# Kernel optimization log

Hardware: AMD Instinct MI355X
Metric: run time of the kernel (lower is better)

The kernel has to match this reference:

```python
import jax, jax.numpy as jnp
import numpy as np

BS, Q, K, NT = 16, 1500, 256, 150   # batch, queries, classes, GT per image (T = BS*NT)
COST_CLASS, COST_BBOX, COST_GIOU = 1.0, 5.0, 2.0
ALPHA, GAMMA, EPS = 0.25, 2.0, 1e-8


def box_cxcywh_to_xyxy(b):
    cx, cy, w, h = b[..., 0], b[..., 1], b[..., 2], b[..., 3]
    return jnp.stack([cx - 0.5 * w, cy - 0.5 * h, cx + 0.5 * w, cy + 0.5 * h], axis=-1)


def generalized_box_iou(boxes1, boxes2):
    # boxes in xyxy; boxes1: [N,4], boxes2: [M,4] -> [N,M]
    area1 = (boxes1[:, 2] - boxes1[:, 0]) * (boxes1[:, 3] - boxes1[:, 1])
    area2 = (boxes2[:, 2] - boxes2[:, 0]) * (boxes2[:, 3] - boxes2[:, 1])
    lt = jnp.maximum(boxes1[:, None, :2], boxes2[None, :, :2])
    rb = jnp.minimum(boxes1[:, None, 2:], boxes2[None, :, 2:])
    wh = jnp.clip(rb - lt, 0.0)
    inter = wh[..., 0] * wh[..., 1]
    union = area1[:, None] + area2[None, :] - inter
    iou = inter / union
    # smallest enclosing box
    lt_e = jnp.minimum(boxes1[:, None, :2], boxes2[None, :, :2])
    rb_e = jnp.maximum(boxes1[:, None, 2:], boxes2[None, :, 2:])
    wh_e = jnp.clip(rb_e - lt_e, 0.0)
    area_e = wh_e[..., 0] * wh_e[..., 1]
    return iou - (area_e - union) / area_e


def setup_inputs() -> dict:
    key = jax.random.key(0)
    k1, k2, k3, k4 = jax.random.split(key, 4)
    pred_logits = jax.random.normal(k1, (BS, Q, K), dtype=jnp.float32)
    pred_boxes = jax.random.uniform(k2, (BS, Q, 4), dtype=jnp.float32, minval=0.05, maxval=0.95)
    tgt_bbox = jax.random.uniform(k3, (BS * NT, 4), dtype=jnp.float32, minval=0.05, maxval=0.95)
    tgt_ids = jax.random.randint(k4, (BS * NT,), 0, K)
    return {"pred_logits": pred_logits, "pred_boxes": pred_boxes,
            "tgt_bbox": tgt_bbox, "tgt_ids": tgt_ids}


def reference(pred_logits, pred_boxes, tgt_bbox, tgt_ids):
    bs, nq, k = pred_logits.shape
    out_prob = jax.nn.sigmoid(pred_logits.reshape(bs * nq, k))   # [N, K]
    out_bbox = pred_boxes.reshape(bs * nq, 4)                    # [N, 4]

    # focal-style classification cost, gathered at target class columns
    neg_cost = (1.0 - ALPHA) * out_prob ** GAMMA * -jnp.log(1.0 - out_prob + EPS)
    pos_cost = ALPHA * (1.0 - out_prob) ** GAMMA * -jnp.log(out_prob + EPS)
    cost_class = (pos_cost - neg_cost)[:, tgt_ids]               # [N, T]

    # L1 box cost (cdist p=1)
    cost_bbox = jnp.sum(jnp.abs(out_bbox[:, None, :] - tgt_bbox[None, :, :]), axis=-1)

    # negative GIoU cost
    cost_giou = -generalized_box_iou(box_cxcywh_to_xyxy(out_bbox),
                                     box_cxcywh_to_xyxy(tgt_bbox))

    C = COST_BBOX * cost_bbox + COST_CLASS * cost_class + COST_GIOU * cost_giou
    return C.reshape(bs, nq, -1)                                  # [bs, Q, T]
```

## Files before the change

kernel.cpp:

```cpp
#include <hip/hip_runtime.h>
#include <cmath>


namespace {
constexpr int kBS = 16, kQ = 1500, kK = 256, kNT = 150;
constexpr int kT  = kBS * kNT;
constexpr int kN  = kBS * kQ;
constexpr int kNPB = 8;
constexpr int kGroups = 3;
constexpr float kAlpha = 0.25f;
constexpr float kEps   = 1e-8f;
}

__global__ __launch_bounds__(256)
void matcher_cost_kernel(const float* __restrict__ logits,
                         const float* __restrict__ pboxes,
                         const float* __restrict__ tboxes,
                         const int*   __restrict__ tids,
                         float* __restrict__ out)
{
    __shared__ float s_cls[kK];
    const int tid = threadIdx.x;
    const int n0  = blockIdx.x * kNPB;

    float tcx[kGroups][4], tcy[kGroups][4], twd[kGroups][4], tht[kGroups][4];
    int   tcl[kGroups][4];
    bool  valid[kGroups];
    const float4* tb4 = reinterpret_cast<const float4*>(tboxes);
    const int4*   ti4 = reinterpret_cast<const int4*>(tids);
#pragma unroll
    for (int g = 0; g < kGroups; ++g) {
        const int q4 = tid + 256 * g;
        valid[g] = (q4 < kT / 4);
        if (valid[g]) {
#pragma unroll
            for (int e = 0; e < 4; ++e) {
                const float4 b = tb4[q4 * 4 + e];
                tcx[g][e] = b.x; tcy[g][e] = b.y; twd[g][e] = b.z; tht[g][e] = b.w;
            }
            const int4 c = ti4[q4];
            tcl[g][0] = c.x; tcl[g][1] = c.y; tcl[g][2] = c.z; tcl[g][3] = c.w;
        }
    }

    for (int i = 0; i < kNPB; ++i) {
        const int n = n0 + i;

        const float x   = logits[n * kK + tid];
        const float p   = __builtin_amdgcn_rcpf(1.0f + __expf(-x));
        const float omp = 1.0f - p;
        const float ccls = -kAlpha * omp * omp * __logf(p + kEps)
                         + (1.0f - kAlpha) * p * p * __logf(omp + kEps);

        __syncthreads();
        s_cls[tid] = ccls;

        const float pcx = pboxes[n * 4 + 0];
        const float pcy = pboxes[n * 4 + 1];
        const float pw  = pboxes[n * 4 + 2];
        const float ph  = pboxes[n * 4 + 3];
        const float px1 = pcx - 0.5f * pw, py1 = pcy - 0.5f * ph;
        const float px2 = pcx + 0.5f * pw, py2 = pcy + 0.5f * ph;
        const float parea = pw * ph;

        __syncthreads();

        float4* orow = reinterpret_cast<float4*>(out + (size_t)n * kT);
#pragma unroll
        for (int g = 0; g < kGroups; ++g) {
            if (!valid[g]) continue;
            float res[4];
#pragma unroll
            for (int e = 0; e < 4; ++e) {
                const float bcx = tcx[g][e], bcy = tcy[g][e];
                const float bw  = twd[g][e], bh  = tht[g][e];

                const float cb = fabsf(pcx - bcx) + fabsf(pcy - bcy)
                               + fabsf(pw - bw)  + fabsf(ph - bh);

                const float tx1 = bcx - 0.5f * bw, ty1 = bcy - 0.5f * bh;
                const float tx2 = bcx + 0.5f * bw, ty2 = bcy + 0.5f * bh;
                const float tarea = bw * bh;
                const float iw = fmaxf(fminf(px2, tx2) - fmaxf(px1, tx1), 0.0f);
                const float ih = fmaxf(fminf(py2, ty2) - fmaxf(py1, ty1), 0.0f);
                const float inter = iw * ih;
                const float uni   = parea + tarea - inter;
                const float ew = fmaxf(fmaxf(px2, tx2) - fminf(px1, tx1), 0.0f);
                const float eh = fmaxf(fmaxf(py2, ty2) - fminf(py1, ty1), 0.0f);
                const float earea = ew * eh;
                const float iou  = inter * __builtin_amdgcn_rcpf(uni);
                const float giou = iou - (earea - uni) * __builtin_amdgcn_rcpf(earea);

                const float cc = s_cls[tcl[g][e]];
                res[e] = 5.0f * cb + cc - 2.0f * giou;
            }
            const float4 v = make_float4(res[0], res[1], res[2], res[3]);
            orow[tid + 256 * g] = v;
        }
    }
}

extern "C" void kernel_launch(void* const* d_in, const int* in_sizes, int n_in,
                              void* d_out, int out_size, void* d_ws, size_t ws_size,
                              hipStream_t stream) {
    const float* logits = (const float*)d_in[0];
    const float* pboxes = (const float*)d_in[1];
    const float* tboxes = (const float*)d_in[2];
    const int*   tids   = (const int*)d_in[3];
    float* out = (float*)d_out;

    dim3 grid(kN / kNPB);
    dim3 block(256);
    hipLaunchKernelGGL(matcher_cost_kernel, grid, block, 0, stream,
                       logits, pboxes, tboxes, tids, out);
}
```

Before: 299.7 us.

## Tile targets into LDS, batch query class costs in fp16, simplify GIoU math

```diff
diff --git a/kernel.cpp b/kernel.cpp
--- a/kernel.cpp
+++ b/kernel.cpp
@@ -1,4 +1,5 @@
 #include <hip/hip_runtime.h>
+#include <hip/hip_fp16.h>
 #include <cmath>
 
 
@@ -6,96 +7,86 @@
 constexpr int kBS = 16, kQ = 1500, kK = 256, kNT = 150;
 constexpr int kT  = kBS * kNT;
 constexpr int kN  = kBS * kQ;
-constexpr int kNPB = 8;
-constexpr int kGroups = 3;
+constexpr int kQB = 16;
+constexpr int kTT = 1024;
+constexpr int kTiles = 3;
 constexpr float kAlpha = 0.25f;
 constexpr float kEps   = 1e-8f;
 }
 
-__global__ __launch_bounds__(256)
+__global__ __launch_bounds__(256, 4)
 void matcher_cost_kernel(const float* __restrict__ logits,
                          const float* __restrict__ pboxes,
                          const float* __restrict__ tboxes,
                          const int*   __restrict__ tids,
                          float* __restrict__ out)
 {
-    __shared__ float s_cls[kK];
-    const int tid = threadIdx.x;
-    const int n0  = blockIdx.x * kNPB;
+    __shared__ float2 s_cxy[kTT];
+    __shared__ float2 s_wh[kTT];
+    __shared__ unsigned char s_cid[kTT];
+    __shared__ __half s_fcl[kQB][kK];
 
-    float tcx[kGroups][4], tcy[kGroups][4], twd[kGroups][4], tht[kGroups][4];
-    int   tcl[kGroups][4];
-    bool  valid[kGroups];
+    const int tid  = threadIdx.x;
+    const int n0   = blockIdx.x * kQB;
+    const int t0   = blockIdx.y * kTT;
+    const int tsz  = min(kTT, kT - t0);
+
     const float4* tb4 = reinterpret_cast<const float4*>(tboxes);
-    const int4*   ti4 = reinterpret_cast<const int4*>(tids);
-#pragma unroll
-    for (int g = 0; g < kGroups; ++g) {
-        const int q4 = tid + 256 * g;
-        valid[g] = (q4 < kT / 4);
-        if (valid[g]) {
-#pragma unroll
-            for (int e = 0; e < 4; ++e) {
-                const float4 b = tb4[q4 * 4 + e];
-                tcx[g][e] = b.x; tcy[g][e] = b.y; twd[g][e] = b.z; tht[g][e] = b.w;
-            }
-            const int4 c = ti4[q4];
-            tcl[g][0] = c.x; tcl[g][1] = c.y; tcl[g][2] = c.z; tcl[g][3] = c.w;
-        }
+    for (int j = tid; j < tsz; j += 256) {
+        const float4 b = tb4[t0 + j];
+        s_cxy[j] = make_float2(b.x, b.y);
+        s_wh[j]  = make_float2(b.z, b.w);
+        s_cid[j] = (unsigned char)tids[t0 + j];
     }
 
-    for (int i = 0; i < kNPB; ++i) {
-        const int n = n0 + i;
-
-        const float x   = logits[n * kK + tid];
+    for (int q = 0; q < kQB; ++q) {
+        const float x   = logits[(n0 + q) * kK + tid];
         const float p   = __builtin_amdgcn_rcpf(1.0f + __expf(-x));
         const float omp = 1.0f - p;
-        const float ccls = -kAlpha * omp * omp * __logf(p + kEps)
-                         + (1.0f - kAlpha) * p * p * __logf(omp + kEps);
+        const float cc  = -kAlpha * omp * omp * __logf(p + kEps)
+                        + (1.0f - kAlpha) * p * p * __logf(omp + kEps);
+        s_fcl[q][tid] = __float2half(cc);
+    }
 
-        __syncthreads();
-        s_cls[tid] = ccls;
+    __syncthreads();
 
+    for (int q = 0; q < kQB; ++q) {
+        const int n = n0 + q;
         const float pcx = pboxes[n * 4 + 0];
         const float pcy = pboxes[n * 4 + 1];
         const float pw  = pboxes[n * 4 + 2];
         const float ph  = pboxes[n * 4 + 3];
-        const float px1 = pcx - 0.5f * pw, py1 = pcy - 0.5f * ph;
-        const float px2 = pcx + 0.5f * pw, py2 = pcy + 0.5f * ph;
+        const float px1 = pcx - 0.5f * pw, px2 = pcx + 0.5f * pw;
+        const float py1 = pcy - 0.5f * ph, py2 = pcy + 0.5f * ph;
         const float parea = pw * ph;
+        float* __restrict__ row = out + (size_t)n * kT + t0;
 
-        __syncthreads();
+        auto body = [&](int t) {
+            const float2 cxy = s_cxy[t];
+            const float2 wh  = s_wh[t];
+            const float bcx = cxy.x, bcy = cxy.y, bw = wh.x, bh = wh.y;
+            const float cc = __half2float(s_fcl[q][s_cid[t]]);
+            const float cb = fabsf(pcx - bcx) + fabsf(pcy - bcy)
+                           + fabsf(pw - bw)  + fabsf(ph - bh);
+            const float tx1 = bcx - 0.5f * bw, tx2 = bcx + 0.5f * bw;
+            const float ty1 = bcy - 0.5f * bh, ty2 = bcy + 0.5f * bh;
+            const float ow = fminf(px2, tx2) - fmaxf(px1, tx1);
+            const float oh = fminf(py2, ty2) - fmaxf(py1, ty1);
+            const float iw = fmaxf(ow, 0.0f), ih = fmaxf(oh, 0.0f);
+            const float ew = (pw + bw) - ow,  eh = (ph + bh) - oh;
+            const float inter = iw * ih;
+            const float uni   = parea + bw * bh - inter;
+            const float earea = ew * eh;
+            const float r    = __builtin_amdgcn_rcpf(uni * earea);
+            const float frac = fmaf(uni, uni, inter * earea) * r;
+            row[t] = fmaf(5.0f, cb, cc + 2.0f) - 2.0f * frac;
+        };
 
-        float4* orow = reinterpret_cast<float4*>(out + (size_t)n * kT);
+        if (tsz == kTT) {
 #pragma unroll
-        for (int g = 0; g < kGroups; ++g) {
-            if (!valid[g]) continue;
-            float res[4];
-#pragma unroll
-            for (int e = 0; e < 4; ++e) {
-                const float bcx = tcx[g][e], bcy = tcy[g][e];
-                const float bw  = twd[g][e], bh  = tht[g][e];
-
-                const float cb = fabsf(pcx - bcx) + fabsf(pcy - bcy)
-                               + fabsf(pw - bw)  + fabsf(ph - bh);
-
-                const float tx1 = bcx - 0.5f * bw, ty1 = bcy - 0.5f * bh;
-                const float tx2 = bcx + 0.5f * bw, ty2 = bcy + 0.5f * bh;
-                const float tarea = bw * bh;
-                const float iw = fmaxf(fminf(px2, tx2) - fmaxf(px1, tx1), 0.0f);
-                const float ih = fmaxf(fminf(py2, ty2) - fmaxf(py1, ty1), 0.0f);
-                const float inter = iw * ih;
-                const float uni   = parea + tarea - inter;
-                const float ew = fmaxf(fmaxf(px2, tx2) - fminf(px1, tx1), 0.0f);
-                const float eh = fmaxf(fmaxf(py2, ty2) - fminf(py1, ty1), 0.0f);
-                const float earea = ew * eh;
-                const float iou  = inter * __builtin_amdgcn_rcpf(uni);
-                const float giou = iou - (earea - uni) * __builtin_amdgcn_rcpf(earea);
-
-                const float cc = s_cls[tcl[g][e]];
-                res[e] = 5.0f * cb + cc - 2.0f * giou;
-            }
-            const float4 v = make_float4(res[0], res[1], res[2], res[3]);
-            orow[tid + 256 * g] = v;
+            for (int e = 0; e < 4; ++e) body(tid + 256 * e);
+        } else {
+            for (int t = tid; t < tsz; t += 256) body(t);
         }
     }
 }
@@ -109,7 +100,7 @@
     const int*   tids   = (const int*)d_in[3];
     float* out = (float*)d_out;
 
-    dim3 grid(kN / kNPB);
+    dim3 grid(kN / kQB, kTiles);
     dim3 block(256);
     hipLaunchKernelGGL(matcher_cost_kernel, grid, block, 0, stream,
                        logits, pboxes, tboxes, tids, out);
```

New measurement: 274.7 us. -8.3%, faster.
